# Kernel optimization log

Measured on AMD Instinct MI355X. Metric: run time of the kernel, lower is better.

Reference implementation:

```python
import jax, jax.numpy as jnp
import numpy as np
import math

B, L, D, H = 8, 512, 512, 8
DH = D // H  # dim per head = 64
ALPHA, BETA = 1.0, 1.0


def setup_inputs() -> dict:
    key = jax.random.key(0)
    ks = jax.random.split(key, 16)
    s = 1.0 / math.sqrt(D)
    sh = 1.0 / math.sqrt(DH)
    return {
        'query': jax.random.normal(ks[0], (B, L, D), jnp.float32),
        'key': jax.random.normal(ks[1], (B, L, D), jnp.float32),
        'value': jax.random.normal(ks[2], (B, L, D), jnp.float32),
        'structure': jax.random.normal(ks[3], (B, L, L, DH), jnp.float32),
        'Wq': jax.random.normal(ks[4], (D, D), jnp.float32) * s,
        'bq': jnp.zeros((D,), jnp.float32),
        'Wk': jax.random.normal(ks[5], (D, D), jnp.float32) * s,
        'bk': jnp.zeros((D,), jnp.float32),
        'Wv': jax.random.normal(ks[6], (D, D), jnp.float32) * s,
        'bv': jnp.zeros((D,), jnp.float32),
        'Wsk': jax.random.normal(ks[7], (DH, DH), jnp.float32) * sh,
        'bsk': jnp.zeros((DH,), jnp.float32),
        'Wsv': jax.random.normal(ks[8], (DH, DH), jnp.float32) * sh,
        'bsv': jnp.zeros((DH,), jnp.float32),
        'Wo': jax.random.normal(ks[9], (D, D), jnp.float32) * s,
        'bo': jnp.zeros((D,), jnp.float32),
    }


def reference(query, key, value, structure, Wq, bq, Wk, bk, Wv, bv,
              Wsk, bsk, Wsv, bsv, Wo, bo):
    # QKV projections -> [B, H, L, DH]
    q = (query @ Wq.T + bq).reshape(B, L, H, DH).transpose(0, 2, 1, 3)
    k = (key @ Wk.T + bk).reshape(B, L, H, DH).transpose(0, 2, 1, 3)
    v = (value @ Wv.T + bv).reshape(B, L, H, DH).transpose(0, 2, 1, 3)
    q = q / math.sqrt(DH)

    # structure projections: [B, Lq, Lk, DH]
    sk = structure @ Wsk.T + bsk
    sv = structure @ Wsv.T + bsv

    # content scores + relation-aware bias
    scores = jnp.einsum('bhqd,bhkd->bhqk', q, k)
    scores = scores + ALPHA * jnp.einsum('bhqd,bqkd->bhqk', q, sk)

    attn = jax.nn.softmax(scores, axis=-1)  # dropout = 0 (eval)

    # context + relation-aware value bias
    ctx = jnp.einsum('bhqk,bhkd->bhqd', attn, v)
    ctx = ctx + BETA * jnp.einsum('bhqk,bqkd->bhqd', attn, sv)

    ctx = ctx.transpose(0, 2, 1, 3).reshape(B, L, D)
    output = ctx @ Wo.T + bo
    first_head_attn = attn[:, 0]  # [B, L, L]
    return output, first_head_attn
```

## Files before the change

kernel.cpp:

```cpp
#include <hip/hip_runtime.h>

#define BB 8
#define LL 512
#define DD 512
#define HH 8
#define DH 64
#define BLD (BB*LL*DD)

typedef _Float16 f16;
typedef f16 f16x8 __attribute__((ext_vector_type(8)));
typedef float f32x4 __attribute__((ext_vector_type(4)));


__device__ inline f16x8 ldg_cvt8(const float* __restrict__ p){
  float4 a = *(const float4*)p;
  float4 b = *(const float4*)(p+4);
  f16x8 r;
  r[0]=(f16)a.x; r[1]=(f16)a.y; r[2]=(f16)a.z; r[3]=(f16)a.w;
  r[4]=(f16)b.x; r[5]=(f16)b.y; r[6]=(f16)b.z; r[7]=(f16)b.w;
  return r;
}
__device__ inline f16x8 ldg_f16x8(const f16* __restrict__ p){ return *(const f16x8*)p; }

template<int MODE>
__global__ __launch_bounds__(256) void gemm_xwT(const float* __restrict__ X,
        const float* __restrict__ W, const float* __restrict__ bias,
        f16* __restrict__ oh, float* __restrict__ of)
{
  int tid = threadIdx.x;
  int w = tid >> 6, lane = tid & 63;
  int l15 = lane & 15, quad = lane >> 4;
  int m0 = blockIdx.x*64 + w*16;
  int n0 = blockIdx.y*64;
  const float* arow = X + (size_t)(m0 + l15)*DD;
  const float* brow[4];
#pragma unroll
  for(int nt=0;nt<4;nt++) brow[nt] = W + (size_t)(n0 + nt*16 + l15)*DD;
  f32x4 acc[4];
#pragma unroll
  for(int nt=0;nt<4;nt++) acc[nt] = (f32x4){0.f,0.f,0.f,0.f};
  for(int ks=0; ks<16; ks++){
    int k0 = ks*32 + quad*8;
    f16x8 a = ldg_cvt8(arow + k0);
#pragma unroll
    for(int nt=0;nt<4;nt++){
      f16x8 b = ldg_cvt8(brow[nt] + k0);
      acc[nt] = __builtin_amdgcn_mfma_f32_16x16x32_f16(a, b, acc[nt], 0,0,0);
    }
  }
#pragma unroll
  for(int nt=0;nt<4;nt++){
    int n = n0 + nt*16 + l15;
    float bb = bias[n];
#pragma unroll
    for(int r=0;r<4;r++){
      int m = m0 + quad*4 + r;
      float v = acc[nt][r] + bb;
      if (MODE==0) v *= 0.125f;
      if (MODE==3){
        of[(size_t)m*DD + n] = v;
      } else {
        int b_ = m >> 9, l = m & 511;
        int h  = n >> 6, e = n & 63;
        size_t idx;
        if (MODE==2) idx = ((size_t)(b_*HH+h)*DH + e)*LL + l;
        else         idx = ((size_t)(b_*HH+h)*LL + l)*DH + e;
        oh[idx] = (f16)v;
      }
    }
  }
}

__global__ __launch_bounds__(256) void qs_kernel(const f16* __restrict__ qh,
        const float* __restrict__ Wsk, f16* __restrict__ qsh)
{
  int row = blockIdx.x*4 + (threadIdx.x>>6);
  int e = threadIdx.x & 63;
  const f16* qr = qh + (size_t)row*DH;
  float acc = 0.f;
#pragma unroll 8
  for(int d=0; d<DH; d++) acc += (float)qr[d] * Wsk[d*DH + e];
  qsh[(size_t)row*DH + e] = (f16)acc;
}

__global__ __launch_bounds__(256) void struct_score(const f16* __restrict__ qsh,
        const float* __restrict__ st, f16* __restrict__ sst)
{
  int w = threadIdx.x >> 6, lane = threadIdx.x & 63;
  int l15 = lane & 15, quad = lane >> 4;
  int qj = blockIdx.x*4 + w;
  int b = blockIdx.y;
  f16x8 aF[2];
#pragma unroll
  for(int ks=0;ks<2;ks++)
    aF[ks] = ldg_f16x8(qsh + ((size_t)(b*HH + (l15&7))*LL + qj)*DH + ks*32 + quad*8);
  const float* sbase = st + ((size_t)b*LL + qj)*LL*DH;
  for(int nt=0; nt<32; nt++){
    int ki0 = nt*16;
    f32x4 acc = (f32x4){0.f,0.f,0.f,0.f};
#pragma unroll
    for(int ks=0;ks<2;ks++){
      f16x8 bF = ldg_cvt8(sbase + (size_t)(ki0 + l15)*DH + ks*32 + quad*8);
      acc = __builtin_amdgcn_mfma_f32_16x16x32_f16(aF[ks], bF, acc, 0,0,0);
    }
    if (quad < 2){
#pragma unroll
      for(int r=0;r<4;r++){
        int h = quad*4 + r;
        sst[((size_t)(b*LL + qj)*HH + h)*LL + ki0 + l15] = (f16)acc[r];
      }
    }
  }
}

__global__ __launch_bounds__(256) void attn_kernel(const f16* __restrict__ qh,
        const f16* __restrict__ kh, const f16* __restrict__ sst, const f16* __restrict__ vth,
        f16* __restrict__ attn, float* __restrict__ ctx, float* __restrict__ out_attn0)
{
  __shared__ f16  plds[4*16*136];
  __shared__ float ldsm[16][4];
  __shared__ float ldsl[16][4];
  __shared__ float clds[4][16][64];
  int w = threadIdx.x>>6, lane = threadIdx.x&63;
  int l15 = lane&15, quad = lane>>4;
  int q0 = blockIdx.x*16, h = blockIdx.y, b = blockIdx.z;

  f16x8 aQ[2];
#pragma unroll
  for(int ks=0;ks<2;ks++)
    aQ[ks] = ldg_f16x8(qh + ((size_t)(b*HH+h)*LL + q0 + l15)*DH + ks*32 + quad*8);

  f32x4 sc[8];
#pragma unroll
  for(int nt=0;nt<8;nt++) sc[nt] = (f32x4){0.f,0.f,0.f,0.f};
  for(int nt=0; nt<8; nt++){
    int ki0 = w*128 + nt*16;
#pragma unroll
    for(int ks=0;ks<2;ks++){
      f16x8 bF = ldg_f16x8(kh + ((size_t)(b*HH+h)*LL + ki0 + l15)*DH + ks*32 + quad*8);
      sc[nt] = __builtin_amdgcn_mfma_f32_16x16x32_f16(aQ[ks], bF, sc[nt], 0,0,0);
    }
  }
#pragma unroll
  for(int nt=0;nt<8;nt++){
#pragma unroll
    for(int r=0;r<4;r++){
      sc[nt][r] += (float)sst[((size_t)(b*LL + q0+quad*4+r)*HH + h)*LL + w*128 + nt*16 + l15];
    }
  }
  float mp[4];
#pragma unroll
  for(int r=0;r<4;r++){
    float m = sc[0][r];
#pragma unroll
    for(int nt=1;nt<8;nt++) m = fmaxf(m, sc[nt][r]);
#pragma unroll
    for(int msk=1;msk<16;msk<<=1) m = fmaxf(m, __shfl_xor(m, msk));
    mp[r] = m;
  }
  if (l15==0){
#pragma unroll
    for(int r=0;r<4;r++) ldsm[quad*4+r][w] = mp[r];
  }
  __syncthreads();
  float mg[4];
#pragma unroll
  for(int r=0;r<4;r++){
    float4 mv = *(const float4*)&ldsm[quad*4+r][0];
    mg[r] = fmaxf(fmaxf(mv.x,mv.y),fmaxf(mv.z,mv.w));
  }
  float lp[4] = {0.f,0.f,0.f,0.f};
#pragma unroll
  for(int nt=0;nt<8;nt++){
#pragma unroll
    for(int r=0;r<4;r++){
      float p = __expf(sc[nt][r]-mg[r]);
      sc[nt][r] = p; lp[r] += p;
    }
  }
#pragma unroll
  for(int r=0;r<4;r++){
#pragma unroll
    for(int msk=1;msk<16;msk<<=1) lp[r] += __shfl_xor(lp[r], msk);
  }
  if (l15==0){
#pragma unroll
    for(int r=0;r<4;r++) ldsl[quad*4+r][w] = lp[r];
  }
  __syncthreads();
  float inv[4];
#pragma unroll
  for(int r=0;r<4;r++){
    float4 lv = *(const float4*)&ldsl[quad*4+r][0];
    inv[r] = 1.f/(lv.x+lv.y+lv.z+lv.w);
  }
  f16* pw = plds + w*2176;
#pragma unroll
  for(int nt=0;nt<8;nt++){
#pragma unroll
    for(int r=0;r<4;r++){
      float a = sc[nt][r]*inv[r];
      int row = quad*4 + r;
      int ki = w*128 + nt*16 + l15;
      attn[((size_t)(b*HH+h)*LL + q0+row)*LL + ki] = (f16)a;
      pw[row*136 + nt*16 + l15] = (f16)a;
      if (h==0) out_attn0[(size_t)(b*LL + q0+row)*LL + ki] = a;
    }
  }
  f32x4 c4[4];
#pragma unroll
  for(int nt=0;nt<4;nt++) c4[nt] = (f32x4){0.f,0.f,0.f,0.f};
#pragma unroll
  for(int ks=0;ks<4;ks++){
    f16x8 aP = *(const f16x8*)&pw[l15*136 + ks*32 + quad*8];
#pragma unroll
    for(int nt=0;nt<4;nt++){
      f16x8 bV = ldg_f16x8(vth + ((size_t)(b*HH+h)*DH + nt*16 + l15)*LL + w*128 + ks*32 + quad*8);
      c4[nt] = __builtin_amdgcn_mfma_f32_16x16x32_f16(aP, bV, c4[nt], 0,0,0);
    }
  }
#pragma unroll
  for(int nt=0;nt<4;nt++){
#pragma unroll
    for(int r=0;r<4;r++) clds[w][quad*4+r][nt*16+l15] = c4[nt][r];
  }
  __syncthreads();
  int t = threadIdx.x;
#pragma unroll
  for(int i=0;i<4;i++){
    int idx = t + i*256;
    int qj = idx>>6, e = idx&63;
    float s = clds[0][qj][e]+clds[1][qj][e]+clds[2][qj][e]+clds[3][qj][e];
    ctx[((size_t)(b*LL + q0+qj))*DD + h*DH + e] = s;
  }
}

__global__ __launch_bounds__(256) void t_ctx_kernel(const f16* __restrict__ attn,
        const float* __restrict__ st, const float* __restrict__ Wsv,
        const float* __restrict__ bsv, float* __restrict__ ctx)
{
  __shared__ f16  stT[4][64*136];
  __shared__ float tl[4][8*64];
  int w = threadIdx.x>>6, lane = threadIdx.x&63;
  int l15 = lane&15, quad = lane>>4;
  int qj = blockIdx.x*4 + w;
  int b = blockIdx.y;
  const float* sbase = st + ((size_t)b*LL + qj)*LL*DH;
  const f16* abase = attn + ((size_t)(b*HH + (l15&7))*LL + qj)*LL;
  f16* myT = stT[w];
  f32x4 tacc[4];
#pragma unroll
  for(int nt=0;nt<4;nt++) tacc[nt] = (f32x4){0.f,0.f,0.f,0.f};

  for(int kt=0; kt<4; kt++){
    int kb = kt*128;
    __syncthreads();
    int e4 = l15*4;
#pragma unroll 4
    for(int i=0;i<32;i++){
      int ki = i*4 + quad;
      float4 v = *(const float4*)(sbase + (size_t)(kb + ki)*DH + e4);
      myT[(e4+0)*136 + ki] = (f16)v.x;
      myT[(e4+1)*136 + ki] = (f16)v.y;
      myT[(e4+2)*136 + ki] = (f16)v.z;
      myT[(e4+3)*136 + ki] = (f16)v.w;
    }
    __syncthreads();
#pragma unroll
    for(int ks=0; ks<4; ks++){
      f16x8 aA = ldg_f16x8(abase + kb + ks*32 + quad*8);
#pragma unroll
      for(int nt=0;nt<4;nt++){
        f16x8 bS = *(const f16x8*)&myT[(nt*16+l15)*136 + ks*32 + quad*8];
        tacc[nt] = __builtin_amdgcn_mfma_f32_16x16x32_f16(aA, bS, tacc[nt], 0,0,0);
      }
    }
  }
  if (quad < 2){
#pragma unroll
    for(int nt=0;nt<4;nt++){
#pragma unroll
      for(int r=0;r<4;r++) tl[w][(quad*4+r)*64 + nt*16 + l15] = tacc[nt][r];
    }
  }
  __syncthreads();
  int d = lane;
  const float4* Wsv4 = (const float4*)Wsv;
  float* base = ctx + ((size_t)(b*LL + qj))*DD;
  float bv = bsv[d];
  for(int h=0; h<8; h++){
    float s2 = 0.f;
#pragma unroll
    for(int q4=0; q4<16; q4++){
      float4 wv = Wsv4[d*16 + q4];
      float4 tt = *(const float4*)&tl[w][h*64 + q4*4];
      s2 += wv.x*tt.x + wv.y*tt.y + wv.z*tt.z + wv.w*tt.w;
    }
    base[h*64 + d] += s2 + bv;
  }
}

extern "C" void kernel_launch(void* const* d_in, const int* in_sizes, int n_in,
                              void* d_out, int out_size, void* d_ws, size_t ws_size,
                              hipStream_t stream)
{
  const float* query = (const float*)d_in[0];
  const float* key   = (const float*)d_in[1];
  const float* value = (const float*)d_in[2];
  const float* st    = (const float*)d_in[3];
  const float* Wq = (const float*)d_in[4];  const float* bq = (const float*)d_in[5];
  const float* Wk = (const float*)d_in[6];  const float* bk = (const float*)d_in[7];
  const float* Wv = (const float*)d_in[8];  const float* bv = (const float*)d_in[9];
  const float* Wsk= (const float*)d_in[10];
  const float* Wsv= (const float*)d_in[12]; const float* bsv= (const float*)d_in[13];
  const float* Wo = (const float*)d_in[14]; const float* bo = (const float*)d_in[15];

  char* ws = (char*)d_ws;
  f16* qh   = (f16*)(ws);
  f16* qsh  = (f16*)(ws + 4194304);
  f16* kh   = (f16*)(ws + 8388608);
  f16* vth  = (f16*)(ws + 12582912);
  f16* sst  = (f16*)(ws + 16777216);
  f16* attn = (f16*)(ws + 50331648);
  float* ctx = (float*)(ws + 83886080);
  float* outp  = (float*)d_out;
  float* attn0 = outp + BLD;

  dim3 blk(256);
  gemm_xwT<0><<<dim3(64,8),blk,0,stream>>>(query, Wq, bq, qh, nullptr);
  gemm_xwT<1><<<dim3(64,8),blk,0,stream>>>(key,   Wk, bk, kh, nullptr);
  gemm_xwT<2><<<dim3(64,8),blk,0,stream>>>(value, Wv, bv, vth, nullptr);
  qs_kernel<<<dim3(8192),blk,0,stream>>>(qh, Wsk, qsh);
  struct_score<<<dim3(128,8),blk,0,stream>>>(qsh, st, sst);
  attn_kernel<<<dim3(32,8,8),blk,0,stream>>>(qh, kh, sst, vth, attn, ctx, attn0);
  t_ctx_kernel<<<dim3(128,8),blk,0,stream>>>(attn, st, Wsv, bsv, ctx);
  gemm_xwT<3><<<dim3(64,8),blk,0,stream>>>(ctx, Wo, bo, nullptr, outp);
}
```

Measured before the change: 1.108 ms.

## Fuse structure-score, softmax, context and structure-value kernels into one pass

Replaces four kernels with a single per-query-row kernel that loads the structure slice once into LDS as f16 and reuses it for both the score bias and the structure-value context. This removes the second full read of the large structure tensor and the global round-trips of the structure-score and attention intermediates. In exchange, the dot products move from MFMA to scalar FMA, every block rereads K and V for all heads, and the large LDS footprint limits occupancy.

```diff
diff --git a/kernel.cpp b/kernel.cpp
--- a/kernel.cpp
+++ b/kernel.cpp
@@ -9,6 +9,7 @@
 
 typedef _Float16 f16;
 typedef f16 f16x8 __attribute__((ext_vector_type(8)));
+typedef f16 f16x4 __attribute__((ext_vector_type(4)));
 typedef float f32x4 __attribute__((ext_vector_type(4)));
 
 
@@ -71,232 +72,186 @@
   }
 }
 
-__global__ __launch_bounds__(256) void qs_kernel(const f16* __restrict__ qh,
-        const float* __restrict__ Wsk, f16* __restrict__ qsh)
+__global__ __launch_bounds__(512, 4) void fused_attn(
+    const f16* __restrict__ qh, const f16* __restrict__ kh, const f16* __restrict__ vth,
+    const float* __restrict__ st, const float* __restrict__ Wsk,
+    const float* __restrict__ Wsv, const float* __restrict__ bsv,
+    float* __restrict__ ctx, float* __restrict__ attn0)
 {
-  int row = blockIdx.x*4 + (threadIdx.x>>6);
-  int e = threadIdx.x & 63;
-  const f16* qr = qh + (size_t)row*DH;
-  float acc = 0.f;
+  __shared__ f16 sS[512*64];
+  __shared__ f16 qrow[8*64];
+  __shared__ f16 qsr[8*64];
+  __shared__ f16 attnl[8*520];
+  __shared__ float redm[64];
+  __shared__ float redl[64];
+  __shared__ float tbuf[8*64];
+
+  const int t = threadIdx.x;
+  const int w = t>>6, l = t&63;
+  const int qj = blockIdx.x, b = blockIdx.y;
+
+  if (t < 64){
+    int h = t>>3, c = t&7;
+    *(f16x8*)&qrow[h*64 + c*8] = ldg_f16x8(qh + ((size_t)(b*HH+h)*LL + qj)*DH + c*8);
+  }
+  const float* sbase = st + ((size_t)b*LL + qj)*(size_t)(LL*DH);
+#pragma unroll
+  for(int i=0;i<8;i++){
+    int idx = t + i*512;
+    int ki = idx>>3, ec = idx&7;
+    const float* p = sbase + ki*64 + ec*8;
+    float4 a = *(const float4*)p;
+    float4 c = *(const float4*)(p+4);
+    f16x8 hv;
+    hv[0]=(f16)a.x; hv[1]=(f16)a.y; hv[2]=(f16)a.z; hv[3]=(f16)a.w;
+    hv[4]=(f16)c.x; hv[5]=(f16)c.y; hv[6]=(f16)c.z; hv[7]=(f16)c.w;
+    *(f16x8*)&sS[ki*64 + ((ec ^ (ki&7))<<3)] = hv;
+  }
+  __syncthreads();
+
+  {
+    float acc = 0.f;
 #pragma unroll 8
-  for(int d=0; d<DH; d++) acc += (float)qr[d] * Wsk[d*DH + e];
-  qsh[(size_t)row*DH + e] = (f16)acc;
-}
-
-__global__ __launch_bounds__(256) void struct_score(const f16* __restrict__ qsh,
-        const float* __restrict__ st, f16* __restrict__ sst)
-{
-  int w = threadIdx.x >> 6, lane = threadIdx.x & 63;
-  int l15 = lane & 15, quad = lane >> 4;
-  int qj = blockIdx.x*4 + w;
-  int b = blockIdx.y;
-  f16x8 aF[2];
-#pragma unroll
-  for(int ks=0;ks<2;ks++)
-    aF[ks] = ldg_f16x8(qsh + ((size_t)(b*HH + (l15&7))*LL + qj)*DH + ks*32 + quad*8);
-  const float* sbase = st + ((size_t)b*LL + qj)*LL*DH;
-  for(int nt=0; nt<32; nt++){
-    int ki0 = nt*16;
-    f32x4 acc = (f32x4){0.f,0.f,0.f,0.f};
-#pragma unroll
-    for(int ks=0;ks<2;ks++){
-      f16x8 bF = ldg_cvt8(sbase + (size_t)(ki0 + l15)*DH + ks*32 + quad*8);
-      acc = __builtin_amdgcn_mfma_f32_16x16x32_f16(aF[ks], bF, acc, 0,0,0);
-    }
-    if (quad < 2){
-#pragma unroll
-      for(int r=0;r<4;r++){
-        int h = quad*4 + r;
-        sst[((size_t)(b*LL + qj)*HH + h)*LL + ki0 + l15] = (f16)acc[r];
-      }
-    }
-  }
-}
-
-__global__ __launch_bounds__(256) void attn_kernel(const f16* __restrict__ qh,
-        const f16* __restrict__ kh, const f16* __restrict__ sst, const f16* __restrict__ vth,
-        f16* __restrict__ attn, float* __restrict__ ctx, float* __restrict__ out_attn0)
-{
-  __shared__ f16  plds[4*16*136];
-  __shared__ float ldsm[16][4];
-  __shared__ float ldsl[16][4];
-  __shared__ float clds[4][16][64];
-  int w = threadIdx.x>>6, lane = threadIdx.x&63;
-  int l15 = lane&15, quad = lane>>4;
-  int q0 = blockIdx.x*16, h = blockIdx.y, b = blockIdx.z;
-
-  f16x8 aQ[2];
-#pragma unroll
-  for(int ks=0;ks<2;ks++)
-    aQ[ks] = ldg_f16x8(qh + ((size_t)(b*HH+h)*LL + q0 + l15)*DH + ks*32 + quad*8);
-
-  f32x4 sc[8];
-#pragma unroll
-  for(int nt=0;nt<8;nt++) sc[nt] = (f32x4){0.f,0.f,0.f,0.f};
-  for(int nt=0; nt<8; nt++){
-    int ki0 = w*128 + nt*16;
-#pragma unroll
-    for(int ks=0;ks<2;ks++){
-      f16x8 bF = ldg_f16x8(kh + ((size_t)(b*HH+h)*LL + ki0 + l15)*DH + ks*32 + quad*8);
-      sc[nt] = __builtin_amdgcn_mfma_f32_16x16x32_f16(aQ[ks], bF, sc[nt], 0,0,0);
-    }
-  }
-#pragma unroll
-  for(int nt=0;nt<8;nt++){
-#pragma unroll
-    for(int r=0;r<4;r++){
-      sc[nt][r] += (float)sst[((size_t)(b*LL + q0+quad*4+r)*HH + h)*LL + w*128 + nt*16 + l15];
-    }
-  }
-  float mp[4];
-#pragma unroll
-  for(int r=0;r<4;r++){
-    float m = sc[0][r];
-#pragma unroll
-    for(int nt=1;nt<8;nt++) m = fmaxf(m, sc[nt][r]);
-#pragma unroll
-    for(int msk=1;msk<16;msk<<=1) m = fmaxf(m, __shfl_xor(m, msk));
-    mp[r] = m;
-  }
-  if (l15==0){
-#pragma unroll
-    for(int r=0;r<4;r++) ldsm[quad*4+r][w] = mp[r];
-  }
-  __syncthreads();
-  float mg[4];
-#pragma unroll
-  for(int r=0;r<4;r++){
-    float4 mv = *(const float4*)&ldsm[quad*4+r][0];
-    mg[r] = fmaxf(fmaxf(mv.x,mv.y),fmaxf(mv.z,mv.w));
-  }
-  float lp[4] = {0.f,0.f,0.f,0.f};
-#pragma unroll
-  for(int nt=0;nt<8;nt++){
-#pragma unroll
-    for(int r=0;r<4;r++){
-      float p = __expf(sc[nt][r]-mg[r]);
-      sc[nt][r] = p; lp[r] += p;
-    }
-  }
-#pragma unroll
-  for(int r=0;r<4;r++){
-#pragma unroll
-    for(int msk=1;msk<16;msk<<=1) lp[r] += __shfl_xor(lp[r], msk);
-  }
-  if (l15==0){
-#pragma unroll
-    for(int r=0;r<4;r++) ldsl[quad*4+r][w] = lp[r];
-  }
-  __syncthreads();
-  float inv[4];
-#pragma unroll
-  for(int r=0;r<4;r++){
-    float4 lv = *(const float4*)&ldsl[quad*4+r][0];
-    inv[r] = 1.f/(lv.x+lv.y+lv.z+lv.w);
-  }
-  f16* pw = plds + w*2176;
-#pragma unroll
-  for(int nt=0;nt<8;nt++){
-#pragma unroll
-    for(int r=0;r<4;r++){
-      float a = sc[nt][r]*inv[r];
-      int row = quad*4 + r;
-      int ki = w*128 + nt*16 + l15;
-      attn[((size_t)(b*HH+h)*LL + q0+row)*LL + ki] = (f16)a;
-      pw[row*136 + nt*16 + l15] = (f16)a;
-      if (h==0) out_attn0[(size_t)(b*LL + q0+row)*LL + ki] = a;
-    }
-  }
-  f32x4 c4[4];
-#pragma unroll
-  for(int nt=0;nt<4;nt++) c4[nt] = (f32x4){0.f,0.f,0.f,0.f};
-#pragma unroll
-  for(int ks=0;ks<4;ks++){
-    f16x8 aP = *(const f16x8*)&pw[l15*136 + ks*32 + quad*8];
-#pragma unroll
-    for(int nt=0;nt<4;nt++){
-      f16x8 bV = ldg_f16x8(vth + ((size_t)(b*HH+h)*DH + nt*16 + l15)*LL + w*128 + ks*32 + quad*8);
-      c4[nt] = __builtin_amdgcn_mfma_f32_16x16x32_f16(aP, bV, c4[nt], 0,0,0);
-    }
-  }
-#pragma unroll
-  for(int nt=0;nt<4;nt++){
-#pragma unroll
-    for(int r=0;r<4;r++) clds[w][quad*4+r][nt*16+l15] = c4[nt][r];
-  }
-  __syncthreads();
-  int t = threadIdx.x;
-#pragma unroll
-  for(int i=0;i<4;i++){
-    int idx = t + i*256;
-    int qj = idx>>6, e = idx&63;
-    float s = clds[0][qj][e]+clds[1][qj][e]+clds[2][qj][e]+clds[3][qj][e];
-    ctx[((size_t)(b*LL + q0+qj))*DD + h*DH + e] = s;
-  }
-}
-
-__global__ __launch_bounds__(256) void t_ctx_kernel(const f16* __restrict__ attn,
-        const float* __restrict__ st, const float* __restrict__ Wsv,
-        const float* __restrict__ bsv, float* __restrict__ ctx)
-{
-  __shared__ f16  stT[4][64*136];
-  __shared__ float tl[4][8*64];
-  int w = threadIdx.x>>6, lane = threadIdx.x&63;
-  int l15 = lane&15, quad = lane>>4;
-  int qj = blockIdx.x*4 + w;
-  int b = blockIdx.y;
-  const float* sbase = st + ((size_t)b*LL + qj)*LL*DH;
-  const f16* abase = attn + ((size_t)(b*HH + (l15&7))*LL + qj)*LL;
-  f16* myT = stT[w];
-  f32x4 tacc[4];
-#pragma unroll
-  for(int nt=0;nt<4;nt++) tacc[nt] = (f32x4){0.f,0.f,0.f,0.f};
-
-  for(int kt=0; kt<4; kt++){
-    int kb = kt*128;
+    for(int y=0;y<64;y++) acc += (float)qrow[w*64+y] * Wsk[y*64 + l];
+    qsr[w*64 + l] = (f16)acc;
+  }
+  __syncthreads();
+
+  const int ki = w*64 + l;
+  const int kx3 = (ki&7)<<3;
+  float s[8];
+#pragma unroll
+  for(int h=0;h<8;h++) s[h]=0.f;
+  const f16* srow = &sS[ki*64];
+  const f16* khb  = kh + (size_t)b*HH*LL*DH + (size_t)ki*DH;
+#pragma unroll
+  for(int ec=0;ec<8;ec++){
+    f16x8 c8 = *(const f16x8*)&srow[(ec<<3) ^ kx3];
+#pragma unroll
+    for(int h=0;h<8;h++){
+      f16x8 k8 = ldg_f16x8(khb + (size_t)h*LL*DH + ec*8);
+      f16x8 q8 = *(const f16x8*)&qrow[h*64 + ec*8];
+      f16x8 g8 = *(const f16x8*)&qsr[h*64 + ec*8];
+      float acc = s[h];
+#pragma unroll
+      for(int j=0;j<8;j++)
+        acc += (float)q8[j]*(float)k8[j] + (float)g8[j]*(float)c8[j];
+      s[h] = acc;
+    }
+  }
+
+  float p[8];
+  {
+#pragma unroll
+    for(int h=0;h<8;h++){
+      float v = s[h];
+#pragma unroll
+      for(int msk=1; msk<64; msk<<=1) v = fmaxf(v, __shfl_xor(v, msk));
+      if (l==0) redm[h*8+w] = v;
+    }
     __syncthreads();
-    int e4 = l15*4;
-#pragma unroll 4
-    for(int i=0;i<32;i++){
-      int ki = i*4 + quad;
-      float4 v = *(const float4*)(sbase + (size_t)(kb + ki)*DH + e4);
-      myT[(e4+0)*136 + ki] = (f16)v.x;
-      myT[(e4+1)*136 + ki] = (f16)v.y;
-      myT[(e4+2)*136 + ki] = (f16)v.z;
-      myT[(e4+3)*136 + ki] = (f16)v.w;
+    float M[8];
+#pragma unroll
+    for(int h=0;h<8;h++){
+      float4 r0 = *(const float4*)&redm[h*8];
+      float4 r1 = *(const float4*)&redm[h*8+4];
+      M[h] = fmaxf(fmaxf(fmaxf(r0.x,r0.y),fmaxf(r0.z,r0.w)),
+                   fmaxf(fmaxf(r1.x,r1.y),fmaxf(r1.z,r1.w)));
+    }
+#pragma unroll
+    for(int h=0;h<8;h++){
+      float v = __expf(s[h]-M[h]);
+      p[h] = v;
+#pragma unroll
+      for(int msk=1; msk<64; msk<<=1) v += __shfl_xor(v, msk);
+      if (l==0) redl[h*8+w] = v;
     }
     __syncthreads();
 #pragma unroll
-    for(int ks=0; ks<4; ks++){
-      f16x8 aA = ldg_f16x8(abase + kb + ks*32 + quad*8);
-#pragma unroll
-      for(int nt=0;nt<4;nt++){
-        f16x8 bS = *(const f16x8*)&myT[(nt*16+l15)*136 + ks*32 + quad*8];
-        tacc[nt] = __builtin_amdgcn_mfma_f32_16x16x32_f16(aA, bS, tacc[nt], 0,0,0);
-      }
-    }
-  }
-  if (quad < 2){
-#pragma unroll
-    for(int nt=0;nt<4;nt++){
-#pragma unroll
-      for(int r=0;r<4;r++) tl[w][(quad*4+r)*64 + nt*16 + l15] = tacc[nt][r];
-    }
-  }
-  __syncthreads();
-  int d = lane;
-  const float4* Wsv4 = (const float4*)Wsv;
-  float* base = ctx + ((size_t)(b*LL + qj))*DD;
-  float bv = bsv[d];
-  for(int h=0; h<8; h++){
-    float s2 = 0.f;
-#pragma unroll
-    for(int q4=0; q4<16; q4++){
-      float4 wv = Wsv4[d*16 + q4];
-      float4 tt = *(const float4*)&tl[w][h*64 + q4*4];
-      s2 += wv.x*tt.x + wv.y*tt.y + wv.z*tt.z + wv.w*tt.w;
-    }
-    base[h*64 + d] += s2 + bv;
+    for(int h=0;h<8;h++){
+      float4 r0 = *(const float4*)&redl[h*8];
+      float4 r1 = *(const float4*)&redl[h*8+4];
+      float tot = (r0.x+r0.y+r0.z+r0.w)+(r1.x+r1.y+r1.z+r1.w);
+      p[h] = p[h] / tot;
+    }
+  }
+#pragma unroll
+  for(int h=0;h<8;h++) attnl[h*520 + ki] = (f16)p[h];
+  attn0[((size_t)(b*LL+qj))*LL + ki] = p[0];
+  __syncthreads();
+
+  float c1a=0.f,c1b=0.f,c1c=0.f,c1d=0.f;
+  const f16* vrow = vth + ((size_t)(b*HH + w)*DH + l)*LL;
+#pragma unroll 16
+  for(int kc=0;kc<64;kc++){
+    f16x8 v8 = ldg_f16x8(vrow + kc*8);
+    f16x8 a8 = *(const f16x8*)&attnl[w*520 + kc*8];
+    c1a += (float)a8[0]*(float)v8[0] + (float)a8[4]*(float)v8[4];
+    c1b += (float)a8[1]*(float)v8[1] + (float)a8[5]*(float)v8[5];
+    c1c += (float)a8[2]*(float)v8[2] + (float)a8[6]*(float)v8[6];
+    c1d += (float)a8[3]*(float)v8[3] + (float)a8[7]*(float)v8[7];
+  }
+  const float c1 = (c1a+c1b)+(c1c+c1d);
+
+  const int q4 = l&15, run = l>>4;
+  const int ki0 = w*64 + run*16;
+  const int ecx = q4>>1, hf = (q4&1)*4;
+  f16x4 sv[16];
+#pragma unroll
+  for(int kk=0;kk<16;kk++){
+    int kia = ki0 + kk;
+    sv[kk] = *(const f16x4*)&sS[kia*64 + ((ecx ^ (kk&7))<<3) + hf];
+  }
+  float ta[8][4];
+#pragma unroll
+  for(int h=0;h<8;h++){ ta[h][0]=0.f; ta[h][1]=0.f; ta[h][2]=0.f; ta[h][3]=0.f; }
+#pragma unroll
+  for(int h=0;h<8;h++){
+    f16x8 a0 = *(const f16x8*)&attnl[h*520 + ki0];
+    f16x8 a1 = *(const f16x8*)&attnl[h*520 + ki0 + 8];
+#pragma unroll
+    for(int kk=0;kk<8;kk++){
+      float av = (float)a0[kk];
+#pragma unroll
+      for(int j=0;j<4;j++) ta[h][j] += av * (float)sv[kk][j];
+    }
+#pragma unroll
+    for(int kk=0;kk<8;kk++){
+      float av = (float)a1[kk];
+#pragma unroll
+      for(int j=0;j<4;j++) ta[h][j] += av * (float)sv[8+kk][j];
+    }
+  }
+  __syncthreads();
+  float* part = (float*)sS;
+  const int g = w*4 + run;
+#pragma unroll
+  for(int h=0;h<8;h++){
+    float4 vv; vv.x=ta[h][0]; vv.y=ta[h][1]; vv.z=ta[h][2]; vv.w=ta[h][3];
+    *(float4*)&part[(size_t)(g*8+h)*64 + q4*4] = vv;
+  }
+  __syncthreads();
+  {
+    float acc2 = 0.f;
+#pragma unroll
+    for(int gg=0; gg<32; gg++) acc2 += part[(size_t)(gg*8+w)*64 + l];
+    tbuf[w*64 + l] = acc2;
+  }
+  __syncthreads();
+
+  {
+    float a3=0.f, b3=0.f;
+    const float4* W4 = (const float4*)(Wsv + l*64);
+#pragma unroll
+    for(int e4=0;e4<16;e4+=2){
+      float4 wv0 = W4[e4];
+      float4 tt0 = *(const float4*)&tbuf[w*64 + e4*4];
+      a3 += wv0.x*tt0.x + wv0.y*tt0.y + wv0.z*tt0.z + wv0.w*tt0.w;
+      float4 wv1 = W4[e4+1];
+      float4 tt1 = *(const float4*)&tbuf[w*64 + e4*4 + 4];
+      b3 += wv1.x*tt1.x + wv1.y*tt1.y + wv1.z*tt1.z + wv1.w*tt1.w;
+    }
+    ctx[((size_t)(b*LL+qj))*DD + w*64 + l] = c1 + (a3+b3) + bsv[l];
   }
 }
 
@@ -317,12 +272,9 @@
 
   char* ws = (char*)d_ws;
   f16* qh   = (f16*)(ws);
-  f16* qsh  = (f16*)(ws + 4194304);
-  f16* kh   = (f16*)(ws + 8388608);
-  f16* vth  = (f16*)(ws + 12582912);
-  f16* sst  = (f16*)(ws + 16777216);
-  f16* attn = (f16*)(ws + 50331648);
-  float* ctx = (float*)(ws + 83886080);
+  f16* kh   = (f16*)(ws + 4194304);
+  f16* vth  = (f16*)(ws + 8388608);
+  float* ctx = (float*)(ws + 12582912);
   float* outp  = (float*)d_out;
   float* attn0 = outp + BLD;
 
@@ -330,9 +282,6 @@
   gemm_xwT<0><<<dim3(64,8),blk,0,stream>>>(query, Wq, bq, qh, nullptr);
   gemm_xwT<1><<<dim3(64,8),blk,0,stream>>>(key,   Wk, bk, kh, nullptr);
   gemm_xwT<2><<<dim3(64,8),blk,0,stream>>>(value, Wv, bv, vth, nullptr);
-  qs_kernel<<<dim3(8192),blk,0,stream>>>(qh, Wsk, qsh);
-  struct_score<<<dim3(128,8),blk,0,stream>>>(qsh, st, sst);
-  attn_kernel<<<dim3(32,8,8),blk,0,stream>>>(qh, kh, sst, vth, attn, ctx, attn0);
-  t_ctx_kernel<<<dim3(128,8),blk,0,stream>>>(attn, st, Wsv, bsv, ctx);
+  fused_attn<<<dim3(512,8), dim3(512), 0, stream>>>(qh, kh, vth, st, Wsk, Wsv, bsv, ctx, attn0);
   gemm_xwT<3><<<dim3(64,8),blk,0,stream>>>(ctx, Wo, bo, nullptr, outp);
 }
```

Result: slower. 4.224 ms (+281.3%).
